# Kernel optimization log

Hardware: AMD Instinct MI355X
Metric: run time of the kernel (lower is better)

Reference implementation:

```python
import jax, jax.numpy as jnp
import numpy as np

D_MODEL = 1024
NUM_HEADS = 16
D_HEAD = D_MODEL // NUM_HEADS
SCALE = float(np.sqrt(D_HEAD))
NEG = -1e9


def setup_inputs() -> dict:
    key = jax.random.key(0)
    ks = jax.random.split(key, 4)
    B, K = 4, 1024
    tokens = jax.random.normal(ks[0], (B, K, D_MODEL), dtype=jnp.float32)
    token_mask = jnp.ones((B, K), dtype=jnp.int32)
    W_qkv = jax.random.normal(ks[1], (D_MODEL, 3 * D_MODEL), dtype=jnp.float32) * 0.02
    b_qkv = jnp.zeros((3 * D_MODEL,), dtype=jnp.float32)
    W_proj = jax.random.normal(ks[2], (D_MODEL, D_MODEL), dtype=jnp.float32) * 0.02
    b_proj = jnp.zeros((D_MODEL,), dtype=jnp.float32)
    return {"tokens": tokens, "token_mask": token_mask, "W_qkv": W_qkv,
            "b_qkv": b_qkv, "W_proj": W_proj, "b_proj": b_proj}


def reference(tokens, token_mask, W_qkv, b_qkv, W_proj, b_proj):
    B, K, D = tokens.shape
    H, dh = NUM_HEADS, D // NUM_HEADS
    # QKV projection: (B, K, 3D) -> (3, B, H, K, dh)
    qkv = (tokens @ W_qkv + b_qkv).reshape(B, K, 3, H, dh)
    qkv = jnp.transpose(qkv, (2, 0, 3, 1, 4))
    q, k, v = qkv[0], qkv[1], qkv[2]
    # scaled scores (B, H, K, K)
    attn = jnp.einsum('bhqd,bhkd->bhqk', q, k) / SCALE
    # additive padding mask: valid iff both query and key positions valid
    tm = token_mask.astype(attn.dtype)
    m = tm[:, None, None, :] * tm[:, None, :, None]          # (B,1,K,K)
    attn = attn + (1.0 - jnp.clip(m, 0.0)) * NEG
    attn = jax.nn.softmax(attn, axis=-1)
    # weighted values, merge heads
    out = jnp.einsum('bhqk,bhkd->bhqd', attn, v)
    out = jnp.transpose(out, (0, 2, 1, 3)).reshape(B, K, D)
    out = out @ W_proj + b_proj
    tokens_out = tokens + out                                 # residual (dropout=0)
    attn_out = attn.mean(axis=1)                              # (B, K, K)
    return tokens_out, attn_out
```

## Files before the change

kernel.cpp:

```cpp
#include <hip/hip_runtime.h>
#include <hip/hip_bf16.h>
#include <math.h>

#define SEQ   1024
#define DM    1024
#define NH    16
#define DH    64
#define INV_SCALE 0.125f
#define NEGBIG   -1e9f
#define MASKPEN 80.0f

typedef __attribute__((ext_vector_type(8))) __bf16 bf16x8;
typedef __attribute__((ext_vector_type(4))) float floatx4;
typedef unsigned short ushort_t;

__device__ __forceinline__ floatx4 mfma16(bf16x8 a, bf16x8 b, floatx4 c) {
    return __builtin_amdgcn_mfma_f32_16x16x32_bf16(a, b, c, 0, 0, 0);
}

__device__ __forceinline__ ushort_t f2bf(float f) {
    unsigned int u = __float_as_uint(f);
    u += 0x7fffu + ((u >> 16) & 1u);
    return (ushort_t)(u >> 16);
}

__device__ __forceinline__ void gload_lds16(const void* g, void* l) {
    __builtin_amdgcn_global_load_lds(
        (const __attribute__((address_space(1))) unsigned int*)g,
        (__attribute__((address_space(3))) unsigned int*)l, 16, 0, 0);
}

__global__ __launch_bounds__(256) void k_prep(const float* __restrict__ tokens,
                                              ushort_t* __restrict__ Xbf,
                                              const float* __restrict__ Wqkv,
                                              ushort_t* __restrict__ Wt,
                                              const float* __restrict__ Wproj,
                                              ushort_t* __restrict__ Wpt) {
    __shared__ ushort_t tile[32][33];
    int bxg = blockIdx.x;
    if (bxg < 2048) {
        int i = (bxg * 256 + threadIdx.x) * 8;
        float4 a = *(const float4*)(tokens + i);
        float4 b = *(const float4*)(tokens + i + 4);
        union { ushort_t s[8]; uint4 v; } pk;
        pk.s[0] = f2bf(a.x); pk.s[1] = f2bf(a.y); pk.s[2] = f2bf(a.z); pk.s[3] = f2bf(a.w);
        pk.s[4] = f2bf(b.x); pk.s[5] = f2bf(b.y); pk.s[6] = f2bf(b.z); pk.s[7] = f2bf(b.w);
        *(uint4*)(Xbf + i) = pk.v;
        return;
    }
    const float* src; ushort_t* dst; int R, C, bx, by;
    if (bxg < 5120) {
        int idx = bxg - 2048;
        src = Wqkv; dst = Wt; R = DM; C = 3 * DM;
        bx = (idx % 96) * 32; by = (idx / 96) * 32;
    } else {
        int idx = bxg - 5120;
        src = Wproj; dst = Wpt; R = DM; C = DM;
        bx = (idx % 32) * 32; by = (idx / 32) * 32;
    }
    int tx = threadIdx.x & 31, ty = threadIdx.x >> 5;
    for (int i = ty; i < 32; i += 8)
        tile[i][tx] = f2bf(src[(size_t)(by + i) * C + bx + tx]);
    __syncthreads();
    for (int i = ty; i < 32; i += 8)
        dst[(size_t)(bx + i) * R + by + tx] = tile[tx][i];
}

__device__ __forceinline__ void gemm128_body(const ushort_t* __restrict__ A,
                                             const ushort_t* __restrict__ Bt,
                                             int m0, int n0, int Kd,
                                             floatx4 acc[4][4], ushort_t* smem) {
    int tid  = threadIdx.x;
    int wave = tid >> 6, lane = tid & 63;
    int l15 = lane & 15, quad = lane >> 4;
    int wr = (wave >> 1) * 64, wc = (wave & 1) * 64;
    int rsub = lane >> 2;
    int ksub = (((lane & 3) ^ ((lane >> 3) & 3)) * 8);
    int rsw  = (l15 >> 1) & 3;

    #pragma unroll
    for (int c = 0; c < 2; ++c) {
        int rbase = wave * 32 + c * 16;
        gload_lds16(A  + (size_t)(m0 + rbase + rsub) * Kd + ksub,
                    smem + rbase * 32);
        gload_lds16(Bt + (size_t)(n0 + rbase + rsub) * Kd + ksub,
                    smem + 4096 + rbase * 32);
    }

    for (int k0 = 0; k0 < Kd; k0 += 32) {
        int sel = (k0 >> 5) & 1;
        ushort_t* cur = smem + sel * 8192;
        __syncthreads();
        if (k0 + 32 < Kd) {
            ushort_t* nxt = smem + (sel ^ 1) * 8192;
            #pragma unroll
            for (int c = 0; c < 2; ++c) {
                int rbase = wave * 32 + c * 16;
                gload_lds16(A  + (size_t)(m0 + rbase + rsub) * Kd + (k0 + 32) + ksub,
                            nxt + rbase * 32);
                gload_lds16(Bt + (size_t)(n0 + rbase + rsub) * Kd + (k0 + 32) + ksub,
                            nxt + 4096 + rbase * 32);
            }
        }

        bf16x8 af[4], bfr[4];
        #pragma unroll
        for (int i = 0; i < 4; ++i)
            af[i] = *(const bf16x8*)(cur + (wr + i * 16 + l15) * 32 + (quad ^ rsw) * 8);
        #pragma unroll
        for (int j = 0; j < 4; ++j)
            bfr[j] = *(const bf16x8*)(cur + 4096 + (wc + j * 16 + l15) * 32 + (quad ^ rsw) * 8);
        #pragma unroll
        for (int i = 0; i < 4; ++i)
            #pragma unroll
            for (int j = 0; j < 4; ++j)
                acc[i][j] = mfma16(af[i], bfr[j], acc[i][j]);
    }
}

__global__ __launch_bounds__(256, 2) void k_qkv_gemm(const ushort_t* __restrict__ X,
                                                     const ushort_t* __restrict__ Wt,
                                                     const float* __restrict__ bias,
                                                     ushort_t* __restrict__ qb,
                                                     ushort_t* __restrict__ kb,
                                                     ushort_t* __restrict__ vtb) {
    __shared__ ushort_t smem[16384];
    int m0 = blockIdx.y * 128, n0 = blockIdx.x * 128;
    floatx4 acc[4][4];
    #pragma unroll
    for (int i = 0; i < 4; ++i)
        #pragma unroll
        for (int j = 0; j < 4; ++j) acc[i][j] = (floatx4)0.0f;

    gemm128_body(X, Wt, m0, n0, DM, acc, smem);

    int tid = threadIdx.x, wave = tid >> 6, lane = tid & 63;
    int l15 = lane & 15, quad = lane >> 4;
    int wr = (wave >> 1) * 64, wc = (wave & 1) * 64;
    #pragma unroll
    for (int i = 0; i < 4; ++i) {
        int mrow0 = m0 + wr + i * 16 + quad * 4;
        int b = mrow0 >> 10, t0 = mrow0 & 1023;
        #pragma unroll
        for (int j = 0; j < 4; ++j) {
            int n = n0 + wc + j * 16 + l15;
            float bv = bias[n];
            int sec = n >> 10, nn = n & 1023;
            int h = nn >> 6, d = nn & 63;
            if (sec == 2) {
                union { ushort_t s[4]; uint2 v; } pk;
                #pragma unroll
                for (int r = 0; r < 4; ++r) pk.s[r] = f2bf(acc[i][j][r] + bv);
                *(uint2*)(vtb + (((size_t)(b * NH + h) * DH + d) * SEQ + t0)) = pk.v;
            } else {
                ushort_t* dst = (sec == 0) ? qb : kb;
                #pragma unroll
                for (int r = 0; r < 4; ++r)
                    dst[((size_t)(b * NH + h) * SEQ + t0 + r) * DH + d] =
                        f2bf(acc[i][j][r] + bv);
            }
        }
    }
}

__global__ __launch_bounds__(256, 4) void k_attn_flash(const ushort_t* __restrict__ qb,
                                                       const ushort_t* __restrict__ kb,
                                                       const ushort_t* __restrict__ vtb,
                                                       const int* __restrict__ mask,
                                                       float* __restrict__ lbuf,
                                                       ushort_t* __restrict__ ob) {
    __shared__ ushort_t ks[2 * 64 * 64];
    __shared__ ushort_t vs[2 * 64 * 64];
    __shared__ ushort_t ps[4 * 16 * 64];
    int bh = blockIdx.x, qt = blockIdx.y;
    int b = bh >> 4, h = bh & 15;
    int tid = threadIdx.x, wave = tid >> 6, lane = tid & 63;
    int l15 = lane & 15, quad = lane >> 4;
    int qrow = qt * 64 + wave * 16;
    ushort_t* pw = ps + wave * 1024;
    int sw7 = l15 & 7;

    int srow = wave * 16 + (lane >> 3);
    int slog = (lane & 7) ^ (srow & 7);

    const ushort_t* qbase = qb + ((size_t)bh * SEQ + qrow + l15) * DH;
    bf16x8 aq0 = *(const bf16x8*)(qbase + quad * 8);
    bf16x8 aq1 = *(const bf16x8*)(qbase + 32 + quad * 8);

    bf16x8 vones;
    #pragma unroll
    for (int i = 0; i < 8; ++i) vones[i] = (__bf16)1.0f;

    float qp[4];
    #pragma unroll
    for (int r = 0; r < 4; ++r)
        qp[r] = MASKPEN * (float)mask[b * SEQ + qrow + quad * 4 + r];

    floatx4 oacc[4], lacc = (floatx4)0.0f;
    #pragma unroll
    for (int t = 0; t < 4; ++t) oacc[t] = (floatx4)0.0f;

    #pragma unroll
    for (int c = 0; c < 2; ++c) {
        gload_lds16(kb  + ((size_t)bh * SEQ + srow + c * 8) * DH + slog * 8,
                    ks + (wave * 16 + c * 8) * 64);
        gload_lds16(vtb + ((size_t)bh * DH + srow + c * 8) * SEQ + slog * 8,
                    vs + (wave * 16 + c * 8) * 64);
    }

    for (int it = 0; it < SEQ / 64; ++it) {
        int kc = it * 64;
        int sel = it & 1;
        __syncthreads();
        if (it + 1 < SEQ / 64) {
            int nsel = sel ^ 1;
            #pragma unroll
            for (int c = 0; c < 2; ++c) {
                gload_lds16(kb  + ((size_t)bh * SEQ + kc + 64 + srow + c * 8) * DH + slog * 8,
                            ks + nsel * 4096 + (wave * 16 + c * 8) * 64);
                gload_lds16(vtb + ((size_t)bh * DH + srow + c * 8) * SEQ + kc + 64 + slog * 8,
                            vs + nsel * 4096 + (wave * 16 + c * 8) * 64);
            }
        }
        const ushort_t* kcur = ks + sel * 4096;
        const ushort_t* vcur = vs + sel * 4096;

        floatx4 s[4];
        #pragma unroll
        for (int j = 0; j < 4; ++j) {
            int row = j * 16 + l15;
            bf16x8 k0 = *(const bf16x8*)(kcur + row * 64 + ((quad ^ sw7) * 8));
            bf16x8 k1 = *(const bf16x8*)(kcur + row * 64 + (((quad + 4) ^ sw7) * 8));
            s[j] = mfma16(aq0, k0, (floatx4)0.0f);
            s[j] = mfma16(aq1, k1, s[j]);
        }
        #pragma unroll
        for (int j = 0; j < 4; ++j) {
            float km = (float)mask[b * SEQ + kc + j * 16 + l15];
            #pragma unroll
            for (int r = 0; r < 4; ++r) {
                float arg = s[j][r] * INV_SCALE + (qp[r] * km - MASKPEN);
                float p = __expf(arg);
                int rd = quad * 4 + r;
                int ch = (2 * j + (l15 >> 3)) ^ (rd & 7);
                pw[rd * 64 + ch * 8 + (l15 & 7)] = f2bf(p);
            }
        }
        bf16x8 pa0 = *(const bf16x8*)(pw + l15 * 64 + ((quad ^ sw7) * 8));
        bf16x8 pa1 = *(const bf16x8*)(pw + l15 * 64 + (((quad + 4) ^ sw7) * 8));
        lacc = mfma16(pa0, vones, lacc);
        lacc = mfma16(pa1, vones, lacc);
        #pragma unroll
        for (int t = 0; t < 4; ++t) {
            bf16x8 bv0 = *(const bf16x8*)(vcur + (t * 16 + l15) * 64 + ((quad ^ sw7) * 8));
            bf16x8 bv1 = *(const bf16x8*)(vcur + (t * 16 + l15) * 64 + (((quad + 4) ^ sw7) * 8));
            oacc[t] = mfma16(pa0, bv0, oacc[t]);
            oacc[t] = mfma16(pa1, bv1, oacc[t]);
        }
    }
    float invl[4];
    #pragma unroll
    for (int r = 0; r < 4; ++r) invl[r] = 1.0f / lacc[r];
    #pragma unroll
    for (int t = 0; t < 4; ++t)
        #pragma unroll
        for (int r = 0; r < 4; ++r)
            ob[((size_t)b * SEQ + qrow + quad * 4 + r) * DM + h * DH + t * 16 + l15] =
                f2bf(oacc[t][r] * invl[r]);
    if (l15 == 0) {
        #pragma unroll
        for (int r = 0; r < 4; ++r)
            lbuf[(size_t)bh * SEQ + qrow + quad * 4 + r] = invl[r];
    }
}

__device__ __forceinline__ void proj_body(const ushort_t* __restrict__ ob,
                                          const ushort_t* __restrict__ Wpt,
                                          const float* __restrict__ bias,
                                          const float* __restrict__ tokens,
                                          float* __restrict__ out,
                                          int m0, int n0, ushort_t* smem) {
    floatx4 acc[4][4];
    #pragma unroll
    for (int i = 0; i < 4; ++i)
        #pragma unroll
        for (int j = 0; j < 4; ++j) acc[i][j] = (floatx4)0.0f;

    gemm128_body(ob, Wpt, m0, n0, DM, acc, smem);

    int tid = threadIdx.x, wave = tid >> 6, lane = tid & 63;
    int l15 = lane & 15, quad = lane >> 4;
    int wr = (wave >> 1) * 64, wc = (wave & 1) * 64;
    #pragma unroll
    for (int i = 0; i < 4; ++i) {
        int m0r = m0 + wr + i * 16 + quad * 4;
        #pragma unroll
        for (int j = 0; j < 4; ++j) {
            int n = n0 + wc + j * 16 + l15;
            float bv = bias[n];
            #pragma unroll
            for (int r = 0; r < 4; ++r) {
                size_t idx = (size_t)(m0r + r) * DM + n;
                out[idx] = acc[i][j][r] + bv + tokens[idx];
            }
        }
    }
}

__device__ __forceinline__ void avg_body(const ushort_t* __restrict__ qb,
                                         const ushort_t* __restrict__ kb,
                                         const int* __restrict__ mask,
                                         const float* __restrict__ lbuf,
                                         float* __restrict__ attn_out,
                                         int bx, ushort_t* ks) {
    int b  = bx >> 8;
    int qt = (bx >> 4) & 15;
    int kt = bx & 15;
    int tid = threadIdx.x, wave = tid >> 6, lane = tid & 63;
    int l15 = lane & 15, quad = lane >> 4;
    int q0 = qt * 64 + wave * 16;
    int kbase = kt * 64;
    int sw7 = l15 & 7;

    int srow = wave * 16 + (lane >> 3);
    int slog = (lane & 7) ^ (srow & 7);
    int bh0 = b * NH;

    float qp[4], km[4];
    #pragma unroll
    for (int r = 0; r < 4; ++r)
        qp[r] = MASKPEN * (float)mask[b * SEQ + q0 + quad * 4 + r];
    #pragma unroll
    for (int j = 0; j < 4; ++j)
        km[j] = (float)mask[b * SEQ + kbase + j * 16 + l15];

    floatx4 aacc[4];
    #pragma unroll
    for (int j = 0; j < 4; ++j) aacc[j] = (floatx4)0.0f;

    #pragma unroll
    for (int c = 0; c < 2; ++c)
        gload_lds16(kb + ((size_t)bh0 * SEQ + kbase + srow + c * 8) * DH + slog * 8,
                    ks + (wave * 16 + c * 8) * 64);
    const ushort_t* qp0 = qb + ((size_t)bh0 * SEQ + q0 + l15) * DH;
    bf16x8 aq0 = *(const bf16x8*)(qp0 + quad * 8);
    bf16x8 aq1 = *(const bf16x8*)(qp0 + 32 + quad * 8);
    floatx4 il = *(const floatx4*)(lbuf + (size_t)bh0 * SEQ + q0 + quad * 4);
    __syncthreads();

    for (int h = 0; h < NH; ++h) {
        ushort_t* cur = ks + (h & 1) * 4096;
        ushort_t* nxt = ks + ((h + 1) & 1) * 4096;
        if (h + 1 < NH) {
            #pragma unroll
            for (int c = 0; c < 2; ++c)
                gload_lds16(kb + ((size_t)(bh0 + h + 1) * SEQ + kbase + srow + c * 8) * DH + slog * 8,
                            nxt + (wave * 16 + c * 8) * 64);
        }
        bf16x8 caq0 = aq0, caq1 = aq1;
        floatx4 cil = il;
        if (h + 1 < NH) {
            const ushort_t* qpn = qb + ((size_t)(bh0 + h + 1) * SEQ + q0 + l15) * DH;
            aq0 = *(const bf16x8*)(qpn + quad * 8);
            aq1 = *(const bf16x8*)(qpn + 32 + quad * 8);
            il = *(const floatx4*)(lbuf + (size_t)(bh0 + h + 1) * SEQ + q0 + quad * 4);
        }
        cil *= 0.0625f;

        #pragma unroll
        for (int j = 0; j < 4; ++j) {
            int row = j * 16 + l15;
            bf16x8 k0 = *(const bf16x8*)(cur + row * 64 + ((quad ^ sw7) * 8));
            bf16x8 k1 = *(const bf16x8*)(cur + row * 64 + (((quad + 4) ^ sw7) * 8));
            floatx4 s = mfma16(caq0, k0, (floatx4)0.0f);
            s = mfma16(caq1, k1, s);
            #pragma unroll
            for (int r = 0; r < 4; ++r) {
                float arg = s[r] * INV_SCALE + (qp[r] * km[j] - MASKPEN);
                aacc[j][r] += __expf(arg) * cil[r];
            }
        }
        __syncthreads();
    }
    #pragma unroll
    for (int j = 0; j < 4; ++j)
        #pragma unroll
        for (int r = 0; r < 4; ++r)
            attn_out[((size_t)b * SEQ + q0 + quad * 4 + r) * SEQ +
                     kbase + j * 16 + l15] = aacc[j][r];
}

__global__ __launch_bounds__(256, 2) void k_proj_avg(const ushort_t* __restrict__ ob,
                                                     const ushort_t* __restrict__ Wpt,
                                                     const float* __restrict__ bias,
                                                     const float* __restrict__ tokens,
                                                     float* __restrict__ out,
                                                     const ushort_t* __restrict__ qb,
                                                     const ushort_t* __restrict__ kb,
                                                     const int* __restrict__ mask,
                                                     const float* __restrict__ lbuf,
                                                     float* __restrict__ attn_out) {
    __shared__ ushort_t smem[16384];
    int bxg = blockIdx.x;
    if (bxg < 256) {
        proj_body(ob, Wpt, bias, tokens, out, (bxg >> 3) * 128, (bxg & 7) * 128, smem);
    } else {
        avg_body(qb, kb, mask, lbuf, attn_out, bxg - 256, smem);
    }
}

__global__ __launch_bounds__(256, 2) void k_proj(const ushort_t* __restrict__ ob,
                                                 const ushort_t* __restrict__ Wpt,
                                                 const float* __restrict__ bias,
                                                 const float* __restrict__ tokens,
                                                 float* __restrict__ out) {
    __shared__ ushort_t smem[16384];
    proj_body(ob, Wpt, bias, tokens, out, blockIdx.y * 128, blockIdx.x * 128, smem);
}

__global__ __launch_bounds__(256, 4) void k_attn_avg(const ushort_t* __restrict__ qb,
                                                     const ushort_t* __restrict__ kb,
                                                     const int* __restrict__ mask,
                                                     const float* __restrict__ lbuf,
                                                     float* __restrict__ attn_out) {
    __shared__ ushort_t ks[2 * 64 * 64];
    avg_body(qb, kb, mask, lbuf, attn_out, blockIdx.x, ks);
}

extern "C" void kernel_launch(void* const* d_in, const int* in_sizes, int n_in,
                              void* d_out, int out_size, void* d_ws, size_t ws_size,
                              hipStream_t stream) {
    const float* tokens = (const float*)d_in[0];
    const int*   mask   = (const int*)d_in[1];
    const float* Wqkv   = (const float*)d_in[2];
    const float* bqkv   = (const float*)d_in[3];
    const float* Wproj  = (const float*)d_in[4];
    const float* bproj  = (const float*)d_in[5];

    float* out_tok  = (float*)d_out;
    float* out_attn = out_tok + (size_t)4 * SEQ * SEQ;

    ushort_t* Wt   = (ushort_t*)d_ws;
    ushort_t* Wpt  = Wt  + (size_t)3 * DM * DM;
    ushort_t* qbuf = Wpt + (size_t)DM * DM;
    ushort_t* kbuf = qbuf + (size_t)4 * SEQ * DM;
    ushort_t* vtb  = kbuf + (size_t)4 * SEQ * DM;
    float*    lbuf = (float*)(vtb + (size_t)4 * SEQ * DM);
    ushort_t* obuf_ws = (ushort_t*)(lbuf + (size_t)4 * NH * SEQ);
    const size_t WS_NEED = 42205184;

    bool big_ws = ws_size >= WS_NEED;
    ushort_t* Xbf  = (ushort_t*)out_attn;
    ushort_t* obuf = big_ws ? obuf_ws
                            : (ushort_t*)(out_attn + (size_t)2 * SEQ * SEQ);

    k_prep<<<6144, 256, 0, stream>>>(tokens, Xbf, Wqkv, Wt, Wproj, Wpt);
    k_qkv_gemm<<<dim3(24, 32), 256, 0, stream>>>(Xbf, Wt, bqkv, qbuf, kbuf, vtb);
    k_attn_flash<<<dim3(64, 16), 256, 0, stream>>>(qbuf, kbuf, vtb, mask, lbuf, obuf);
    if (big_ws) {
        k_proj_avg<<<256 + 1024, 256, 0, stream>>>(obuf, Wpt, bproj, tokens, out_tok,
                                                   qbuf, kbuf, mask, lbuf, out_attn);
    } else {
        k_proj<<<dim3(8, 32), 256, 0, stream>>>(obuf, Wpt, bproj, tokens, out_tok);
        k_attn_avg<<<1024, 256, 0, stream>>>(qbuf, kbuf, mask, lbuf, out_attn);
    }
}
```

Measured before the change: 202.7 us.

## Load K fragments directly into registers instead of staging through LDS

```diff
diff --git a/kernel.cpp b/kernel.cpp
--- a/kernel.cpp
+++ b/kernel.cpp
@@ -307,12 +307,41 @@
     }
 }
 
+__device__ __forceinline__ void loadK(bf16x8 dst[8], const ushort_t* __restrict__ kB,
+                                      int h, int l15, int quad) {
+    const ushort_t* p = kB + (size_t)h * SEQ * DH + l15 * DH + quad * 8;
+    #pragma unroll
+    for (int j = 0; j < 4; ++j) {
+        dst[2 * j]     = *(const bf16x8*)(p + j * 16 * DH);
+        dst[2 * j + 1] = *(const bf16x8*)(p + j * 16 * DH + 32);
+    }
+}
+
+__device__ __forceinline__ void headAcc(const bf16x8 kf[8], const ushort_t* __restrict__ qB,
+                                        const float* __restrict__ lB, int h,
+                                        const float qp[4], const float km[4],
+                                        floatx4 aacc[4]) {
+    const ushort_t* qh = qB + (size_t)h * SEQ * DH;
+    bf16x8 a0 = *(const bf16x8*)(qh);
+    bf16x8 a1 = *(const bf16x8*)(qh + 32);
+    floatx4 il = *(const floatx4*)(lB + (size_t)h * SEQ);
+    il *= 0.0625f;
+    #pragma unroll
+    for (int j = 0; j < 4; ++j) {
+        floatx4 s = mfma16(a0, kf[2 * j], (floatx4)0.0f);
+        s = mfma16(a1, kf[2 * j + 1], s);
+        #pragma unroll
+        for (int r = 0; r < 4; ++r)
+            aacc[j][r] += __expf(s[r] * INV_SCALE + (qp[r] * km[j] - MASKPEN)) * il[r];
+    }
+}
+
 __device__ __forceinline__ void avg_body(const ushort_t* __restrict__ qb,
                                          const ushort_t* __restrict__ kb,
                                          const int* __restrict__ mask,
                                          const float* __restrict__ lbuf,
                                          float* __restrict__ attn_out,
-                                         int bx, ushort_t* ks) {
+                                         int bx) {
     int b  = bx >> 8;
     int qt = (bx >> 4) & 15;
     int kt = bx & 15;
@@ -320,10 +349,6 @@
     int l15 = lane & 15, quad = lane >> 4;
     int q0 = qt * 64 + wave * 16;
     int kbase = kt * 64;
-    int sw7 = l15 & 7;
-
-    int srow = wave * 16 + (lane >> 3);
-    int slog = (lane & 7) ^ (srow & 7);
     int bh0 = b * NH;
 
     float qp[4], km[4];
@@ -338,50 +363,19 @@
     #pragma unroll
     for (int j = 0; j < 4; ++j) aacc[j] = (floatx4)0.0f;
 
-    #pragma unroll
-    for (int c = 0; c < 2; ++c)
-        gload_lds16(kb + ((size_t)bh0 * SEQ + kbase + srow + c * 8) * DH + slog * 8,
-                    ks + (wave * 16 + c * 8) * 64);
-    const ushort_t* qp0 = qb + ((size_t)bh0 * SEQ + q0 + l15) * DH;
-    bf16x8 aq0 = *(const bf16x8*)(qp0 + quad * 8);
-    bf16x8 aq1 = *(const bf16x8*)(qp0 + 32 + quad * 8);
-    floatx4 il = *(const floatx4*)(lbuf + (size_t)bh0 * SEQ + q0 + quad * 4);
-    __syncthreads();
-
-    for (int h = 0; h < NH; ++h) {
-        ushort_t* cur = ks + (h & 1) * 4096;
-        ushort_t* nxt = ks + ((h + 1) & 1) * 4096;
-        if (h + 1 < NH) {
-            #pragma unroll
-            for (int c = 0; c < 2; ++c)
-                gload_lds16(kb + ((size_t)(bh0 + h + 1) * SEQ + kbase + srow + c * 8) * DH + slog * 8,
-                            nxt + (wave * 16 + c * 8) * 64);
-        }
-        bf16x8 caq0 = aq0, caq1 = aq1;
-        floatx4 cil = il;
-        if (h + 1 < NH) {
-            const ushort_t* qpn = qb + ((size_t)(bh0 + h + 1) * SEQ + q0 + l15) * DH;
-            aq0 = *(const bf16x8*)(qpn + quad * 8);
-            aq1 = *(const bf16x8*)(qpn + 32 + quad * 8);
-            il = *(const floatx4*)(lbuf + (size_t)(bh0 + h + 1) * SEQ + q0 + quad * 4);
-        }
-        cil *= 0.0625f;
-
-        #pragma unroll
-        for (int j = 0; j < 4; ++j) {
-            int row = j * 16 + l15;
-            bf16x8 k0 = *(const bf16x8*)(cur + row * 64 + ((quad ^ sw7) * 8));
-            bf16x8 k1 = *(const bf16x8*)(cur + row * 64 + (((quad + 4) ^ sw7) * 8));
-            floatx4 s = mfma16(caq0, k0, (floatx4)0.0f);
-            s = mfma16(caq1, k1, s);
-            #pragma unroll
-            for (int r = 0; r < 4; ++r) {
-                float arg = s[r] * INV_SCALE + (qp[r] * km[j] - MASKPEN);
-                aacc[j][r] += __expf(arg) * cil[r];
-            }
-        }
-        __syncthreads();
-    }
+    const ushort_t* kB = kb + ((size_t)bh0 * SEQ + kbase) * DH;
+    const ushort_t* qB = qb + ((size_t)bh0 * SEQ + q0 + l15) * DH + quad * 8;
+    const float*    lB = lbuf + (size_t)bh0 * SEQ + q0 + quad * 4;
+
+    bf16x8 kban0[8], kban1[8];
+    loadK(kban0, kB, 0, l15, quad);
+    for (int h = 0; h < NH; h += 2) {
+        loadK(kban1, kB, h + 1, l15, quad);
+        headAcc(kban0, qB, lB, h, qp, km, aacc);
+        if (h + 2 < NH) loadK(kban0, kB, h + 2, l15, quad);
+        headAcc(kban1, qB, lB, h + 1, qp, km, aacc);
+    }
+
     #pragma unroll
     for (int j = 0; j < 4; ++j)
         #pragma unroll
@@ -405,7 +399,7 @@
     if (bxg < 256) {
         proj_body(ob, Wpt, bias, tokens, out, (bxg >> 3) * 128, (bxg & 7) * 128, smem);
     } else {
-        avg_body(qb, kb, mask, lbuf, attn_out, bxg - 256, smem);
+        avg_body(qb, kb, mask, lbuf, attn_out, bxg - 256);
     }
 }
 
@@ -423,8 +417,7 @@
                                                      const int* __restrict__ mask,
                                                      const float* __restrict__ lbuf,
                                                      float* __restrict__ attn_out) {
-    __shared__ ushort_t ks[2 * 64 * 64];
-    avg_body(qb, kb, mask, lbuf, attn_out, blockIdx.x, ks);
+    avg_body(qb, kb, mask, lbuf, attn_out, blockIdx.x);
 }
 
 extern "C" void kernel_launch(void* const* d_in, const int* in_sizes, int n_in,
```

Result: slower. 240.8 us (+18.8%).
